# Performance work log

Measured on AMD Instinct MI355X. Metric: run time of the kernel, lower is better.

Reference implementation:

```python
import jax, jax.numpy as jnp
import numpy as np

HEADS = 16
D_MODEL = 1024
HEAD_DIM = D_MODEL // HEADS


def setup_inputs() -> dict:
    key = jax.random.key(0)
    ks = jax.random.split(key, 11)
    B, S, D = 2, 2048, D_MODEL
    s = 1.0 / np.sqrt(D)
    inp = {
        'Q': jax.random.normal(ks[0], (B, S, D), jnp.float32),
        'K': jax.random.normal(ks[1], (B, S, D), jnp.float32),
        'V': jax.random.normal(ks[2], (B, S, D), jnp.float32),
        'Wq': jax.random.normal(ks[3], (D, D), jnp.float32) * s,
        'Wk': jax.random.normal(ks[4], (D, D), jnp.float32) * s,
        'Wv': jax.random.normal(ks[5], (D, D), jnp.float32) * s,
        'Wo': jax.random.normal(ks[6], (D, D), jnp.float32) * s,
        'bq': jnp.zeros((D,), jnp.float32),
        'bk': jnp.zeros((D,), jnp.float32),
        'bv': jnp.zeros((D,), jnp.float32),
        'bo': jnp.zeros((D,), jnp.float32),
    }
    return inp


def reference(Q, K, V, Wq, Wk, Wv, Wo, bq, bk, bv, bo):
    B, S, D = Q.shape
    H, Dh = HEADS, HEAD_DIM
    # projections (torch Linear: x @ W.T + b)
    q = (Q @ Wq.T + bq).reshape(B, S, H, Dh).transpose(0, 2, 1, 3)  # [B,H,S,Dh]
    k = (K @ Wk.T + bk).reshape(B, S, H, Dh).transpose(0, 2, 1, 3)
    v = (V @ Wv.T + bv).reshape(B, S, H, Dh).transpose(0, 2, 1, 3)
    # naive scaled dot-product attention, scale = 1/sqrt(head_dim)
    scores = jnp.einsum('bhqd,bhkd->bhqk', q, k) / jnp.sqrt(jnp.float32(Dh))
    attn = jax.nn.softmax(scores, axis=-1)
    out = jnp.einsum('bhqk,bhkd->bhqd', attn, v)
    concat = out.transpose(0, 2, 1, 3).reshape(B, S, D)
    return concat @ Wo.T + bo
```

## Files before the change

kernel.cpp:

```cpp
#include <hip/hip_runtime.h>
#include <hip/hip_bf16.h>


#define SEQ     2048
#define DMODEL  1024
#define NHEADS  16
#define DH      64
#define MROWS   4096
#define M1      (1024*1024)
#define M4      (4*1024*1024)
#define SCQ     0.18033688f

typedef __hip_bfloat16 bf16;
typedef __attribute__((ext_vector_type(8))) short  short8;
typedef __attribute__((ext_vector_type(4))) float  f32x4;

__device__ __forceinline__ bf16 f2b(float x) { return __float2bfloat16(x); }
__device__ __forceinline__ float u2f(unsigned short u) {
    union { unsigned int i; float f; } x; x.i = ((unsigned int)u) << 16; return x.f;
}
__device__ __forceinline__ f32x4 mfma16(short8 a, short8 b, f32x4 c) {
    return __builtin_amdgcn_mfma_f32_16x16x32_bf16(a, b, c, 0, 0, 0);
}
__device__ __forceinline__ unsigned pk2(float a, float b) {
    union { __hip_bfloat162 h; unsigned u; } x;
    x.h = __float22bfloat162_rn(float2{a, b});
    return x.u;
}
__device__ __forceinline__ short8 pk8(float4 a, float4 b) {
    union { short8 s; unsigned u[4]; } x;
    x.u[0] = pk2(a.x, a.y); x.u[1] = pk2(a.z, a.w);
    x.u[2] = pk2(b.x, b.y); x.u[3] = pk2(b.z, b.w);
    return x.s;
}
__device__ __forceinline__ float fexp2(float x) {
    return __builtin_amdgcn_exp2f(x);
}
#define GLDS(g, l) __builtin_amdgcn_global_load_lds( \
    (const __attribute__((address_space(1))) void*)(g), \
    (__attribute__((address_space(3))) void*)(l), 16, 0, 0)

__global__ __launch_bounds__(256) void cvt_all(
    const float* __restrict__ Wq, const float* __restrict__ Wk,
    const float* __restrict__ Wv, const float* __restrict__ Wo,
    const float* __restrict__ Q,  const float* __restrict__ K,
    const float* __restrict__ V,  bf16* __restrict__ dst)
{
    const size_t gid = (size_t)blockIdx.x * 256 + threadIdx.x;
    const size_t e0 = gid * 8;
    const float* s;
    if (e0 < (size_t)4 * M1) {
        const float* w[4] = {Wq, Wk, Wv, Wo};
        s = w[e0 >> 20] + (e0 & (M1 - 1));
    } else {
        const float* a[4] = {nullptr, Q, K, V};
        s = a[e0 >> 22] + (e0 & (M4 - 1));
    }
    float4 x = *(const float4*)s, y = *(const float4*)(s + 4);
    *(short8*)((short*)dst + e0) = pk8(x, y);
}

__global__ __launch_bounds__(256) void cvt_w(
    const float* __restrict__ W0, const float* __restrict__ W1,
    const float* __restrict__ W2, const float* __restrict__ W3,
    bf16* __restrict__ dst)
{
    const int gid = blockIdx.x * 256 + threadIdx.x;
    const int t   = gid >> 17;
    const int off = (gid & 131071) * 8;
    const float* srcs[4] = {W0, W1, W2, W3};
    const float* s = srcs[t] + off;
    float4 a = *(const float4*)s, b = *(const float4*)(s + 4);
    *(short8*)((short*)dst + (size_t)gid * 8) = pk8(a, b);
}

__global__ __launch_bounds__(256) void cvt_1(
    const float* __restrict__ X, bf16* __restrict__ D)
{
    const int gid = blockIdx.x * 256 + threadIdx.x;
    const int off = gid * 8;
    float4 a = *(const float4*)(X + off), b = *(const float4*)(X + off + 4);
    *(short8*)((short*)D + off) = pk8(a, b);
}

template <int BN>
__device__ __forceinline__ void gemm_body(
    const bf16* __restrict__ A, const bf16* __restrict__ B,
    const float* __restrict__ bias, void* __restrict__ outp,
    int m0, int n0, int mode, int bias_m, float scale)
{
    __shared__ short As[128 * 32];
    __shared__ short Bs[BN * 32];
    constexpr int NI = BN / 32;

    const int tid  = threadIdx.x;
    const int lane = tid & 63;
    const int wv   = tid >> 6;
    const int wm   = (wv >> 1) * 64;
    const int wn   = (wv & 1) * (BN / 2);
    const int fn   = lane & 15;
    const int fq   = lane >> 4;

    const int srow = lane >> 2;
    const int scol = (lane & 3) * 8;

    const short* Ag = (const short*)A;
    const short* Bg = (const short*)B;

    f32x4 acc[4][NI];
#pragma unroll
    for (int i = 0; i < 4; ++i)
#pragma unroll
        for (int j = 0; j < NI; ++j) acc[i][j] = (f32x4){0.f, 0.f, 0.f, 0.f};

    for (int k0 = 0; k0 < DMODEL; k0 += 32) {
#pragma unroll
        for (int i = 0; i < 2; ++i) {
            const int rr = wv * 32 + i * 16;
            const short* ga = Ag + (size_t)(m0 + rr + srow) * DMODEL + k0 + scol;
            GLDS(ga, As + rr * 32);
        }
#pragma unroll
        for (int i = 0; i < BN / 64; ++i) {
            const int rr = wv * (BN / 4) + i * 16;
            const short* gb = Bg + (size_t)(n0 + rr + srow) * DMODEL + k0 + scol;
            GLDS(gb, Bs + rr * 32);
        }
        __syncthreads();

        short8 af[4], bfr[NI];
#pragma unroll
        for (int im = 0; im < 4; ++im)
            af[im] = *(const short8*)(As + (wm + im * 16 + fn) * 32 + fq * 8);
#pragma unroll
        for (int in = 0; in < NI; ++in)
            bfr[in] = *(const short8*)(Bs + (wn + in * 16 + fn) * 32 + fq * 8);
#pragma unroll
        for (int im = 0; im < 4; ++im)
#pragma unroll
            for (int in = 0; in < NI; ++in)
                acc[im][in] = mfma16(af[im], bfr[in], acc[im][in]);
        __syncthreads();
    }

#pragma unroll
    for (int im = 0; im < 4; ++im) {
#pragma unroll
        for (int in = 0; in < NI; ++in) {
#pragma unroll
            for (int r = 0; r < 4; ++r) {
                const int m = m0 + wm + im * 16 + fq * 4 + r;
                const int n = n0 + wn + in * 16 + fn;
                const float c = (acc[im][in][r] + (bias_m ? bias[m] : bias[n])) * scale;
                if (mode == 0) {
                    ((float*)outp)[(size_t)m * DMODEL + n] = c;
                } else if (mode == 1) {
                    const int b = m >> 11, s = m & (SEQ - 1);
                    const int h = n >> 6,  d = n & (DH - 1);
                    ((bf16*)outp)[(((size_t)(b * NHEADS + h) * SEQ) + s) * DH + d] = f2b(c);
                } else {
                    const int h = m >> 6,  d = m & (DH - 1);
                    const int b = n >> 11, s = n & (SEQ - 1);
                    const int p = s & 31;
                    const int sp = (s & ~31) | ((p & 12) << 1) | ((p & 16) >> 2) | (p & 3);
                    ((bf16*)outp)[(((size_t)(b * NHEADS + h) * DH) + d) * SEQ + sp] = f2b(c);
                }
            }
        }
    }
}

__global__ __launch_bounds__(256, 3) void gemm_one(
    const bf16* A, const bf16* B, const float* bias, void* out,
    int mode, int bias_m, float scale)
{
    gemm_body<128>(A, B, bias, out, blockIdx.x * 128, blockIdx.y * 128,
                   mode, bias_m, scale);
}

__global__ __launch_bounds__(256, 3) void gemm_fin(
    const bf16* A, const bf16* B, const float* bias, void* out)
{
    gemm_body<64>(A, B, bias, out, blockIdx.x * 128, blockIdx.y * 64, 0, 0, 1.f);
}

__global__ __launch_bounds__(256, 3) void gemm_qkv(
    const bf16* Qb, const bf16* Kb, const bf16* Vb, const bf16* Wb,
    const float* bq, const float* bk, const float* bv,
    bf16* qp, bf16* kp, bf16* vp)
{
    const int blk = blockIdx.x;
    const int z = blk >> 8, t = blk & 255;
    if (z == 0)
        gemm_body<128>(Qb, Wb,          bq, qp, (t >> 3) * 128, (t & 7) * 128, 1, 0, SCQ);
    else if (z == 1)
        gemm_body<128>(Kb, Wb + M1,     bk, kp, (t >> 3) * 128, (t & 7) * 128, 1, 0, 1.f);
    else
        gemm_body<128>(Wb + 2 * M1, Vb, bv, vp, (t >> 5) * 128, (t & 31) * 128, 2, 1, 1.f);
}

__global__ __launch_bounds__(512, 4) void attn_fused(
    const bf16* __restrict__ q,
    const bf16* __restrict__ k,
    const bf16* __restrict__ vt,
    bf16* __restrict__ out)
{
    __shared__ short LB[32768];

    const int tid  = threadIdx.x;
    const int wave = tid >> 6;
    const int half = wave >> 2;
    const int w4   = wave & 3;
    const int lane = tid & 63;
    const int n    = lane & 15;
    const int quad = lane >> 4;

    const int blk  = blockIdx.x;
    const int xcd  = blk & 7;
    const int rest = blk >> 3;
    const int qt   = rest & 15;
    const int bh   = ((rest >> 4) << 3) | xcd;
    const int q0w  = qt * 128 + w4 * 32;
    const int kt0  = half * 16;

    const bf16* qhead = q  + (size_t)bh * SEQ * DH;
    const bf16* khead = k  + (size_t)bh * SEQ * DH;
    const bf16* vhead = vt + (size_t)bh * DH * SEQ;

    short* Kb0 = LB + half * 16384;
    short* Vb0 = LB + half * 16384 + 8192;

    short8 qf[2][2];
#pragma unroll
    for (int qg = 0; qg < 2; ++qg) {
        const short* qr = (const short*)(qhead + (size_t)(q0w + qg * 16 + n) * DH);
        qf[qg][0] = *(const short8*)(qr + quad * 8);
        qf[qg][1] = *(const short8*)(qr + 32 + quad * 8);
    }

    const short8 onesv = {(short)0x3F80, (short)0x3F80, (short)0x3F80, (short)0x3F80,
                          (short)0x3F80, (short)0x3F80, (short)0x3F80, (short)0x3F80};
    const f32x4 Zv = (f32x4){0.f, 0.f, 0.f, 0.f};

    f32x4 O[4][2];
#pragma unroll
    for (int gd = 0; gd < 4; ++gd)
#pragma unroll
        for (int qg = 0; qg < 2; ++qg) O[gd][qg] = Zv;
    f32x4 lacc[2][2] = {{Zv, Zv}, {Zv, Zv}};

    const int srow = lane >> 3;
    const int schk = (lane & 7) ^ srow;
    const int off0 = ((quad       ^ (n & 7)) * 8);
    const int off1 = (((4 + quad) ^ (n & 7)) * 8);

    auto stage = [&](int kt, int buf) {
        const int kbase = kt * 64;
#pragma unroll
        for (int i = 0; i < 2; ++i) {
            const int r = w4 * 16 + i * 8 + srow;
            const char* gk = (const char*)(khead + (size_t)(kbase + r) * DH) + schk * 16;
            const char* gv = (const char*)(vhead + (size_t)r * SEQ + kbase) + schk * 16;
            GLDS(gk, Kb0 + buf * 4096 + (w4 * 16 + i * 8) * 64);
            GLDS(gv, Vb0 + buf * 4096 + (w4 * 16 + i * 8) * 64);
        }
    };

    auto tile_body = [&](const short* KtB, const short* VtB) {
        f32x4 st[4][2];
#pragma unroll
        for (int g = 0; g < 4; ++g) {
            const short* kr = KtB + (g * 16 + n) * 64;
            short8 kf0 = *(const short8*)(kr + off0);
            short8 kf1 = *(const short8*)(kr + off1);
#pragma unroll
            for (int qg = 0; qg < 2; ++qg) {
                f32x4 s = mfma16(kf0, qf[qg][0], Zv);
                s = mfma16(kf1, qf[qg][1], s);
                st[g][qg] = s;
            }
        }
        short8 bP[2][2];
#pragma unroll
        for (int t = 0; t < 2; ++t) {
#pragma unroll
            for (int qg = 0; qg < 2; ++qg) {
                union { short8 s8; unsigned u[4]; } bb;
                bb.u[0] = pk2(fexp2(st[2*t][qg][0]),   fexp2(st[2*t][qg][1]));
                bb.u[1] = pk2(fexp2(st[2*t][qg][2]),   fexp2(st[2*t][qg][3]));
                bb.u[2] = pk2(fexp2(st[2*t+1][qg][0]), fexp2(st[2*t+1][qg][1]));
                bb.u[3] = pk2(fexp2(st[2*t+1][qg][2]), fexp2(st[2*t+1][qg][3]));
                bP[t][qg] = bb.s8;
                lacc[t][qg] = mfma16(onesv, bP[t][qg], lacc[t][qg]);
            }
        }
#pragma unroll
        for (int gd = 0; gd < 4; ++gd) {
            const short* vr = VtB + (gd * 16 + n) * 64;
            short8 vf0 = *(const short8*)(vr + off0);
            short8 vf1 = *(const short8*)(vr + off1);
#pragma unroll
            for (int qg = 0; qg < 2; ++qg) {
                O[gd][qg] = mfma16(vf0, bP[0][qg], O[gd][qg]);
                O[gd][qg] = mfma16(vf1, bP[1][qg], O[gd][qg]);
            }
        }
    };

    stage(kt0, 0);
#pragma unroll 1
    for (int t = 0; t < 16; t += 2) {
        __syncthreads();
        stage(kt0 + t + 1, 1);
        tile_body(Kb0, Vb0);
        __syncthreads();
        if (t + 2 < 16) stage(kt0 + t + 2, 0);
        tile_body(Kb0 + 4096, Vb0 + 4096);
    }

    float* scr = (float*)LB + (size_t)(w4 * 64 + lane) * 34;
    const float l0 = lacc[0][0][0] + lacc[1][0][0];
    const float l1 = lacc[0][1][0] + lacc[1][1][0];

    __syncthreads();
    if (half == 1) {
#pragma unroll
        for (int gd = 0; gd < 4; ++gd)
#pragma unroll
            for (int qg = 0; qg < 2; ++qg) {
                *(float2*)(scr + (gd * 2 + qg) * 4)     = float2{O[gd][qg][0], O[gd][qg][1]};
                *(float2*)(scr + (gd * 2 + qg) * 4 + 2) = float2{O[gd][qg][2], O[gd][qg][3]};
            }
        *(float2*)(scr + 32) = float2{l0, l1};
    }
    __syncthreads();
    if (half == 0) {
        const float2 lo = *(const float2*)(scr + 32);
        const float inv0 = 1.0f / (l0 + lo.x);
        const float inv1 = 1.0f / (l1 + lo.y);
        const int b = bh >> 4;
        const int h = bh & (NHEADS - 1);
#pragma unroll
        for (int gd = 0; gd < 4; ++gd) {
#pragma unroll
            for (int qg = 0; qg < 2; ++qg) {
                const float iv = qg ? inv1 : inv0;
                float2 a = *(const float2*)(scr + (gd * 2 + qg) * 4);
                float2 c = *(const float2*)(scr + (gd * 2 + qg) * 4 + 2);
                const int s = q0w + qg * 16 + n;
                uint2 o;
                o.x = pk2((O[gd][qg][0] + a.x) * iv, (O[gd][qg][1] + a.y) * iv);
                o.y = pk2((O[gd][qg][2] + c.x) * iv, (O[gd][qg][3] + c.y) * iv);
                *(uint2*)(out + ((size_t)(b * SEQ + s)) * DMODEL + h * DH + gd * 16 + quad * 4) = o;
            }
        }
    }
}

__global__ __launch_bounds__(256) void attn_mfma(
    const bf16* __restrict__ q,
    const bf16* __restrict__ k,
    const bf16* __restrict__ vt,
    bf16* __restrict__ out)
{
    __shared__ short Kt[2][64 * 64];
    __shared__ short Vt[2][64 * 64];

    const int tid  = threadIdx.x;
    const int wave = tid >> 6;
    const int lane = tid & 63;
    const int n    = lane & 15;
    const int quad = lane >> 4;

    const int blk  = blockIdx.x;
    const int xcd  = blk & 7;
    const int rest = blk >> 3;
    const int qt   = rest & 15;
    const int bh   = ((rest >> 4) << 3) | xcd;
    const int q0w  = qt * 128 + wave * 32;

    const bf16* qhead = q  + (size_t)bh * SEQ * DH;
    const bf16* khead = k  + (size_t)bh * SEQ * DH;
    const bf16* vhead = vt + (size_t)bh * DH * SEQ;

    short8 qf[2][2];
#pragma unroll
    for (int qg = 0; qg < 2; ++qg) {
        const short* qr = (const short*)(qhead + (size_t)(q0w + qg * 16 + n) * DH);
        qf[qg][0] = *(const short8*)(qr + quad * 8);
        qf[qg][1] = *(const short8*)(qr + 32 + quad * 8);
    }

    const short8 onesv = {(short)0x3F80, (short)0x3F80, (short)0x3F80, (short)0x3F80,
                          (short)0x3F80, (short)0x3F80, (short)0x3F80, (short)0x3F80};
    const f32x4 Zv = (f32x4){0.f, 0.f, 0.f, 0.f};

    f32x4 O[4][2];
#pragma unroll
    for (int gd = 0; gd < 4; ++gd)
#pragma unroll
        for (int qg = 0; qg < 2; ++qg) O[gd][qg] = Zv;
    f32x4 lacc[2] = {Zv, Zv};

    const int srow = lane >> 3;
    const int schk = (lane & 7) ^ srow;
    const int off0 = ((quad       ^ (n & 7)) * 8);
    const int off1 = (((4 + quad) ^ (n & 7)) * 8);

    auto stage = [&](int kt, int buf) {
        const int kbase = kt * 64;
#pragma unroll
        for (int i = 0; i < 2; ++i) {
            const int r = wave * 16 + i * 8 + srow;
            const char* gk = (const char*)(khead + (size_t)(kbase + r) * DH) + schk * 16;
            const char* gv = (const char*)(vhead + (size_t)r * SEQ + kbase) + schk * 16;
            GLDS(gk, Kt[buf] + (wave * 16 + i * 8) * 64);
            GLDS(gv, Vt[buf] + (wave * 16 + i * 8) * 64);
        }
    };

    auto tile_body = [&](const short* KtB, const short* VtB) {
        f32x4 st[4][2];
#pragma unroll
        for (int g = 0; g < 4; ++g) {
            const short* kr = KtB + (g * 16 + n) * 64;
            short8 kf0 = *(const short8*)(kr + off0);
            short8 kf1 = *(const short8*)(kr + off1);
#pragma unroll
            for (int qg = 0; qg < 2; ++qg) {
                f32x4 s = mfma16(kf0, qf[qg][0], Zv);
                s = mfma16(kf1, qf[qg][1], s);
                st[g][qg] = s;
            }
        }
        short8 bP[2][2];
#pragma unroll
        for (int t = 0; t < 2; ++t) {
#pragma unroll
            for (int qg = 0; qg < 2; ++qg) {
                union { short8 s8; unsigned u[4]; } bb;
                bb.u[0] = pk2(fexp2(st[2*t][qg][0]),   fexp2(st[2*t][qg][1]));
                bb.u[1] = pk2(fexp2(st[2*t][qg][2]),   fexp2(st[2*t][qg][3]));
                bb.u[2] = pk2(fexp2(st[2*t+1][qg][0]), fexp2(st[2*t+1][qg][1]));
                bb.u[3] = pk2(fexp2(st[2*t+1][qg][2]), fexp2(st[2*t+1][qg][3]));
                bP[t][qg] = bb.s8;
                lacc[qg] = mfma16(onesv, bP[t][qg], lacc[qg]);
            }
        }
#pragma unroll
        for (int gd = 0; gd < 4; ++gd) {
            const short* vr = VtB + (gd * 16 + n) * 64;
            short8 vf0 = *(const short8*)(vr + off0);
            short8 vf1 = *(const short8*)(vr + off1);
#pragma unroll
            for (int qg = 0; qg < 2; ++qg) {
                O[gd][qg] = mfma16(vf0, bP[0][qg], O[gd][qg]);
                O[gd][qg] = mfma16(vf1, bP[1][qg], O[gd][qg]);
            }
        }
    };

    stage(0, 0);
#pragma unroll 1
    for (int kt = 0; kt < SEQ / 64; kt += 2) {
        __syncthreads();
        stage(kt + 1, 1);
        tile_body(Kt[0], Vt[0]);
        __syncthreads();
        if (kt + 2 < SEQ / 64) stage(kt + 2, 0);
        tile_body(Kt[1], Vt[1]);
    }

    const float inv0 = 1.0f / lacc[0][0];
    const float inv1 = 1.0f / lacc[1][0];
    const int b = bh >> 4;
    const int h = bh & (NHEADS - 1);
#pragma unroll
    for (int gd = 0; gd < 4; ++gd) {
#pragma unroll
        for (int qg = 0; qg < 2; ++qg) {
            const float iv = qg ? inv1 : inv0;
            const int s = q0w + qg * 16 + n;
            uint2 o;
            o.x = pk2(O[gd][qg][0] * iv, O[gd][qg][1] * iv);
            o.y = pk2(O[gd][qg][2] * iv, O[gd][qg][3] * iv);
            *(uint2*)(out + ((size_t)(b * SEQ + s)) * DMODEL + h * DH + gd * 16 + quad * 4) = o;
        }
    }
}

extern "C" void kernel_launch(void* const* d_in, const int* in_sizes, int n_in,
                              void* d_out, int out_size, void* d_ws, size_t ws_size,
                              hipStream_t stream) {
    const float* Q  = (const float*)d_in[0];
    const float* K  = (const float*)d_in[1];
    const float* V  = (const float*)d_in[2];
    const float* Wq = (const float*)d_in[3];
    const float* Wk = (const float*)d_in[4];
    const float* Wv = (const float*)d_in[5];
    const float* Wo = (const float*)d_in[6];
    const float* bq = (const float*)d_in[7];
    const float* bk = (const float*)d_in[8];
    const float* bv = (const float*)d_in[9];
    const float* bo = (const float*)d_in[10];

    bf16* kp = (bf16*)d_out;
    bf16* vp = kp + M4;

    dim3 bb(256);
    dim3 gqk(MROWS / 128, DMODEL / 128);
    dim3 gvv(DMODEL / 128, MROWS / 128);
    dim3 gfin(MROWS / 128, DMODEL / 64);

    if (ws_size >= (size_t)40 * 1024 * 1024) {
        bf16* Wb = (bf16*)d_ws;
        bf16* Qb = Wb + 4 * M1;
        bf16* Kb = Qb + M4;
        bf16* Vb = Kb + M4;
        bf16* qp = Vb + M4;
        bf16* ao = Qb;

        cvt_all<<<8192, bb, 0, stream>>>(Wq, Wk, Wv, Wo, Q, K, V, Wb);
        gemm_qkv<<<768, bb, 0, stream>>>(Qb, Kb, Vb, Wb, bq, bk, bv, qp, kp, vp);
        attn_fused<<<512, 512, 0, stream>>>(qp, kp, vp, ao);
        gemm_fin<<<gfin, bb, 0, stream>>>(ao, Wb + 3 * M1, bo, d_out);
    } else {
        bf16* Wb = (bf16*)d_ws;
        bf16* Xb = Wb + 4 * M1;
        bf16* qp = Xb + M4;
        bf16* ao = Xb;

        cvt_w<<<2048, bb, 0, stream>>>(Wq, Wk, Wv, Wo, Wb);
        cvt_1<<<2048, bb, 0, stream>>>(Q, Xb);
        gemm_one<<<gqk, bb, 0, stream>>>(Xb, Wb, bq, qp, 1, 0, SCQ);
        cvt_1<<<2048, bb, 0, stream>>>(K, Xb);
        gemm_one<<<gqk, bb, 0, stream>>>(Xb, Wb + M1, bk, kp, 1, 0, 1.f);
        cvt_1<<<2048, bb, 0, stream>>>(V, Xb);
        gemm_one<<<gvv, bb, 0, stream>>>(Wb + 2 * M1, Xb, bv, vp, 2, 1, 1.f);
        attn_mfma<<<512, bb, 0, stream>>>(qp, kp, vp, ao);
        gemm_fin<<<gfin, bb, 0, stream>>>(ao, Wb + 3 * M1, bo, d_out);
    }
}
```

Before: 211.9 us.

## Software-pipeline attention loop: overlap QK/exp of next tile with PV of previous

Splits K and V staging into separate async loads and restructures the attention inner loop so that the QK^T and exp2 step for tile t runs alongside the PV and row-sum MFMAs for tile t-1. V is now fetched one stage later than K, with a prologue and epilogue to fill and drain the pipeline. The aim is to interleave the transcendental and pack work with MFMA work and to hide load latency. In exchange it keeps two sets of P fragments live, which raises register pressure and may lower occupancy.

```diff
diff --git a/kernel.cpp b/kernel.cpp
--- a/kernel.cpp
+++ b/kernel.cpp
@@ -16,9 +16,6 @@
 typedef __attribute__((ext_vector_type(4))) float  f32x4;
 
 __device__ __forceinline__ bf16 f2b(float x) { return __float2bfloat16(x); }
-__device__ __forceinline__ float u2f(unsigned short u) {
-    union { unsigned int i; float f; } x; x.i = ((unsigned int)u) << 16; return x.f;
-}
 __device__ __forceinline__ f32x4 mfma16(short8 a, short8 b, f32x4 c) {
     return __builtin_amdgcn_mfma_f32_16x16x32_bf16(a, b, c, 0, 0, 0);
 }
@@ -254,45 +251,61 @@
     const int off0 = ((quad       ^ (n & 7)) * 8);
     const int off1 = (((4 + quad) ^ (n & 7)) * 8);
 
-    auto stage = [&](int kt, int buf) {
+    auto stageK = [&](int kt, int buf) {
         const int kbase = kt * 64;
 #pragma unroll
         for (int i = 0; i < 2; ++i) {
             const int r = w4 * 16 + i * 8 + srow;
             const char* gk = (const char*)(khead + (size_t)(kbase + r) * DH) + schk * 16;
+            GLDS(gk, Kb0 + buf * 4096 + (w4 * 16 + i * 8) * 64);
+        }
+    };
+    auto stageV = [&](int kt, int buf) {
+        const int kbase = kt * 64;
+#pragma unroll
+        for (int i = 0; i < 2; ++i) {
+            const int r = w4 * 16 + i * 8 + srow;
             const char* gv = (const char*)(vhead + (size_t)r * SEQ + kbase) + schk * 16;
-            GLDS(gk, Kb0 + buf * 4096 + (w4 * 16 + i * 8) * 64);
             GLDS(gv, Vb0 + buf * 4096 + (w4 * 16 + i * 8) * 64);
         }
     };
 
-    auto tile_body = [&](const short* KtB, const short* VtB) {
-        f32x4 st[4][2];
-#pragma unroll
-        for (int g = 0; g < 4; ++g) {
-            const short* kr = KtB + (g * 16 + n) * 64;
-            short8 kf0 = *(const short8*)(kr + off0);
-            short8 kf1 = *(const short8*)(kr + off1);
-#pragma unroll
-            for (int qg = 0; qg < 2; ++qg) {
-                f32x4 s = mfma16(kf0, qf[qg][0], Zv);
-                s = mfma16(kf1, qf[qg][1], s);
-                st[g][qg] = s;
-            }
-        }
-        short8 bP[2][2];
-#pragma unroll
-        for (int t = 0; t < 2; ++t) {
+    auto xph = [&](int t, short8 (&bPc)[2][2]) {
+        const short* KtB = Kb0 + (t & 1) * 4096;
+#pragma unroll
+        for (int tt = 0; tt < 2; ++tt) {
+            f32x4 st[2][2];
+#pragma unroll
+            for (int g2 = 0; g2 < 2; ++g2) {
+                const int g = tt * 2 + g2;
+                const short* kr = KtB + (g * 16 + n) * 64;
+                short8 kf0 = *(const short8*)(kr + off0);
+                short8 kf1 = *(const short8*)(kr + off1);
+#pragma unroll
+                for (int qg = 0; qg < 2; ++qg) {
+                    f32x4 s = mfma16(kf0, qf[qg][0], Zv);
+                    s = mfma16(kf1, qf[qg][1], s);
+                    st[g2][qg] = s;
+                }
+            }
 #pragma unroll
             for (int qg = 0; qg < 2; ++qg) {
                 union { short8 s8; unsigned u[4]; } bb;
-                bb.u[0] = pk2(fexp2(st[2*t][qg][0]),   fexp2(st[2*t][qg][1]));
-                bb.u[1] = pk2(fexp2(st[2*t][qg][2]),   fexp2(st[2*t][qg][3]));
-                bb.u[2] = pk2(fexp2(st[2*t+1][qg][0]), fexp2(st[2*t+1][qg][1]));
-                bb.u[3] = pk2(fexp2(st[2*t+1][qg][2]), fexp2(st[2*t+1][qg][3]));
-                bP[t][qg] = bb.s8;
-                lacc[t][qg] = mfma16(onesv, bP[t][qg], lacc[t][qg]);
-            }
+                bb.u[0] = pk2(fexp2(st[0][qg][0]), fexp2(st[0][qg][1]));
+                bb.u[1] = pk2(fexp2(st[0][qg][2]), fexp2(st[0][qg][3]));
+                bb.u[2] = pk2(fexp2(st[1][qg][0]), fexp2(st[1][qg][1]));
+                bb.u[3] = pk2(fexp2(st[1][qg][2]), fexp2(st[1][qg][3]));
+                bPc[tt][qg] = bb.s8;
+            }
+        }
+    };
+
+    auto yph = [&](int t, short8 (&bPp)[2][2]) {
+        const short* VtB = Vb0 + (t & 1) * 4096;
+#pragma unroll
+        for (int qg = 0; qg < 2; ++qg) {
+            lacc[0][qg] = mfma16(onesv, bPp[0][qg], lacc[0][qg]);
+            lacc[1][qg] = mfma16(onesv, bPp[1][qg], lacc[1][qg]);
         }
 #pragma unroll
         for (int gd = 0; gd < 4; ++gd) {
@@ -301,22 +314,40 @@
             short8 vf1 = *(const short8*)(vr + off1);
 #pragma unroll
             for (int qg = 0; qg < 2; ++qg) {
-                O[gd][qg] = mfma16(vf0, bP[0][qg], O[gd][qg]);
-                O[gd][qg] = mfma16(vf1, bP[1][qg], O[gd][qg]);
+                O[gd][qg] = mfma16(vf0, bPp[0][qg], O[gd][qg]);
+                O[gd][qg] = mfma16(vf1, bPp[1][qg], O[gd][qg]);
             }
         }
     };
 
-    stage(kt0, 0);
+    short8 bPA[2][2], bPB[2][2];
+
+    stageK(kt0, 0);
+
+    __syncthreads();
+    stageK(kt0 + 1, 1);
+    stageV(kt0, 0);
+    xph(0, bPA);
+
 #pragma unroll 1
-    for (int t = 0; t < 16; t += 2) {
+    for (int t = 1; t < 15; t += 2) {
         __syncthreads();
-        stage(kt0 + t + 1, 1);
-        tile_body(Kb0, Vb0);
+        stageK(kt0 + t + 1, (t + 1) & 1);
+        stageV(kt0 + t, t & 1);
+        xph(t, bPB);
+        yph(t - 1, bPA);
         __syncthreads();
-        if (t + 2 < 16) stage(kt0 + t + 2, 0);
-        tile_body(Kb0 + 4096, Vb0 + 4096);
-    }
+        stageK(kt0 + t + 2, (t + 2) & 1);
+        stageV(kt0 + t + 1, (t + 1) & 1);
+        xph(t + 1, bPA);
+        yph(t, bPB);
+    }
+    __syncthreads();
+    stageV(kt0 + 15, 1);
+    xph(15, bPB);
+    yph(14, bPA);
+    __syncthreads();
+    yph(15, bPB);
 
     float* scr = (float*)LB + (size_t)(w4 * 64 + lane) * 34;
     const float l0 = lacc[0][0][0] + lacc[1][0][0];
```

Measured after the change: 225.7 us. 6.5% more time.

## Load K/V tiles straight into registers instead of staging through LDS

Applied to the files above, without the earlier changes.

The attention kernel stops staging K and V tiles into shared memory with global_load_lds and double buffering. Each wave now loads its own K/V fragments from global memory into registers and prefetches the next tile while the current one is computed, which removes the per-tile __syncthreads and LDS traffic. Shared memory shrinks to the small reduction scratch buffer, and the occupancy hint in launch_bounds drops from 4 to 2 blocks per CU. In exchange, K/V data that waves used to share through LDS is fetched redundantly by every wave from global memory or cache, and register pressure rises.

```diff
diff --git a/kernel.cpp b/kernel.cpp
--- a/kernel.cpp
+++ b/kernel.cpp
@@ -16,9 +16,6 @@
 typedef __attribute__((ext_vector_type(4))) float  f32x4;
 
 __device__ __forceinline__ bf16 f2b(float x) { return __float2bfloat16(x); }
-__device__ __forceinline__ float u2f(unsigned short u) {
-    union { unsigned int i; float f; } x; x.i = ((unsigned int)u) << 16; return x.f;
-}
 __device__ __forceinline__ f32x4 mfma16(short8 a, short8 b, f32x4 c) {
     return __builtin_amdgcn_mfma_f32_16x16x32_bf16(a, b, c, 0, 0, 0);
 }
@@ -199,13 +196,13 @@
         gemm_body<128>(Wb + 2 * M1, Vb, bv, vp, (t >> 5) * 128, (t & 31) * 128, 2, 1, 1.f);
 }
 
-__global__ __launch_bounds__(512, 4) void attn_fused(
+__global__ __launch_bounds__(512, 2) void attn_fused(
     const bf16* __restrict__ q,
     const bf16* __restrict__ k,
     const bf16* __restrict__ vt,
     bf16* __restrict__ out)
 {
-    __shared__ short LB[32768];
+    __shared__ float SCR[256 * 34];
 
     const int tid  = threadIdx.x;
     const int wave = tid >> 6;
@@ -223,19 +220,18 @@
     const int q0w  = qt * 128 + w4 * 32;
     const int kt0  = half * 16;
 
-    const bf16* qhead = q  + (size_t)bh * SEQ * DH;
-    const bf16* khead = k  + (size_t)bh * SEQ * DH;
-    const bf16* vhead = vt + (size_t)bh * DH * SEQ;
-
-    short* Kb0 = LB + half * 16384;
-    short* Vb0 = LB + half * 16384 + 8192;
-
-    short8 qf[2][2];
-#pragma unroll
-    for (int qg = 0; qg < 2; ++qg) {
-        const short* qr = (const short*)(qhead + (size_t)(q0w + qg * 16 + n) * DH);
-        qf[qg][0] = *(const short8*)(qr + quad * 8);
-        qf[qg][1] = *(const short8*)(qr + 32 + quad * 8);
+    const short* qh = (const short*)(q  + (size_t)bh * SEQ * DH);
+    const short* kh = (const short*)(k  + (size_t)bh * SEQ * DH);
+    const short* vh = (const short*)(vt + (size_t)bh * DH * SEQ);
+
+    short8 qf00, qf01, qf10, qf11;
+    {
+        const short* qr0 = qh + (size_t)(q0w + n) * DH;
+        qf00 = *(const short8*)(qr0 + quad * 8);
+        qf01 = *(const short8*)(qr0 + 32 + quad * 8);
+        const short* qr1 = qh + (size_t)(q0w + 16 + n) * DH;
+        qf10 = *(const short8*)(qr1 + quad * 8);
+        qf11 = *(const short8*)(qr1 + 32 + quad * 8);
     }
 
     const short8 onesv = {(short)0x3F80, (short)0x3F80, (short)0x3F80, (short)0x3F80,
@@ -247,80 +243,86 @@
     for (int gd = 0; gd < 4; ++gd)
 #pragma unroll
         for (int qg = 0; qg < 2; ++qg) O[gd][qg] = Zv;
-    f32x4 lacc[2][2] = {{Zv, Zv}, {Zv, Zv}};
-
-    const int srow = lane >> 3;
-    const int schk = (lane & 7) ^ srow;
-    const int off0 = ((quad       ^ (n & 7)) * 8);
-    const int off1 = (((4 + quad) ^ (n & 7)) * 8);
-
-    auto stage = [&](int kt, int buf) {
-        const int kbase = kt * 64;
-#pragma unroll
-        for (int i = 0; i < 2; ++i) {
-            const int r = w4 * 16 + i * 8 + srow;
-            const char* gk = (const char*)(khead + (size_t)(kbase + r) * DH) + schk * 16;
-            const char* gv = (const char*)(vhead + (size_t)r * SEQ + kbase) + schk * 16;
-            GLDS(gk, Kb0 + buf * 4096 + (w4 * 16 + i * 8) * 64);
-            GLDS(gv, Vb0 + buf * 4096 + (w4 * 16 + i * 8) * 64);
-        }
-    };
-
-    auto tile_body = [&](const short* KtB, const short* VtB) {
+    f32x4 lc0 = Zv, lc1 = Zv;
+
+    const short* kp[4];
+    const short* vp[4];
+#pragma unroll
+    for (int g = 0; g < 4; ++g)
+        kp[g] = kh + (size_t)(kt0 * 64 + g * 16 + n) * 64 + quad * 8;
+#pragma unroll
+    for (int gd = 0; gd < 4; ++gd)
+        vp[gd] = vh + (size_t)(gd * 16 + n) * SEQ + kt0 * 64 + quad * 8;
+
+    short8 Kr[4][2];
+    short8 Vr[4][2];
+
+#pragma unroll
+    for (int g = 0; g < 4; ++g) {
+        Kr[g][0] = *(const short8*)(kp[g]);
+        Kr[g][1] = *(const short8*)(kp[g] + 32);
+    }
+#pragma unroll
+    for (int gd = 0; gd < 4; ++gd) {
+        Vr[gd][0] = *(const short8*)(vp[gd]);
+        Vr[gd][1] = *(const short8*)(vp[gd] + 32);
+    }
+
+#pragma unroll 1
+    for (int t = 0; t < 16; ++t) {
         f32x4 st[4][2];
 #pragma unroll
         for (int g = 0; g < 4; ++g) {
-            const short* kr = KtB + (g * 16 + n) * 64;
-            short8 kf0 = *(const short8*)(kr + off0);
-            short8 kf1 = *(const short8*)(kr + off1);
-#pragma unroll
-            for (int qg = 0; qg < 2; ++qg) {
-                f32x4 s = mfma16(kf0, qf[qg][0], Zv);
-                s = mfma16(kf1, qf[qg][1], s);
-                st[g][qg] = s;
-            }
-        }
-        short8 bP[2][2];
-#pragma unroll
-        for (int t = 0; t < 2; ++t) {
+            f32x4 s0 = mfma16(Kr[g][0], qf00, Zv);
+            st[g][0] = mfma16(Kr[g][1], qf01, s0);
+            f32x4 s1 = mfma16(Kr[g][0], qf10, Zv);
+            st[g][1] = mfma16(Kr[g][1], qf11, s1);
+        }
+        if (t < 15) {
+#pragma unroll
+            for (int g = 0; g < 4; ++g) {
+                kp[g] += 64 * 64;
+                Kr[g][0] = *(const short8*)(kp[g]);
+                Kr[g][1] = *(const short8*)(kp[g] + 32);
+            }
+        }
+        short8 P[2][2];
+#pragma unroll
+        for (int tt = 0; tt < 2; ++tt) {
 #pragma unroll
             for (int qg = 0; qg < 2; ++qg) {
                 union { short8 s8; unsigned u[4]; } bb;
-                bb.u[0] = pk2(fexp2(st[2*t][qg][0]),   fexp2(st[2*t][qg][1]));
-                bb.u[1] = pk2(fexp2(st[2*t][qg][2]),   fexp2(st[2*t][qg][3]));
-                bb.u[2] = pk2(fexp2(st[2*t+1][qg][0]), fexp2(st[2*t+1][qg][1]));
-                bb.u[3] = pk2(fexp2(st[2*t+1][qg][2]), fexp2(st[2*t+1][qg][3]));
-                bP[t][qg] = bb.s8;
-                lacc[t][qg] = mfma16(onesv, bP[t][qg], lacc[t][qg]);
-            }
-        }
+                bb.u[0] = pk2(fexp2(st[2*tt][qg][0]),   fexp2(st[2*tt][qg][1]));
+                bb.u[1] = pk2(fexp2(st[2*tt][qg][2]),   fexp2(st[2*tt][qg][3]));
+                bb.u[2] = pk2(fexp2(st[2*tt+1][qg][0]), fexp2(st[2*tt+1][qg][1]));
+                bb.u[3] = pk2(fexp2(st[2*tt+1][qg][2]), fexp2(st[2*tt+1][qg][3]));
+                P[tt][qg] = bb.s8;
+            }
+        }
+        lc0 = mfma16(onesv, P[0][0], lc0);
+        lc1 = mfma16(onesv, P[0][1], lc1);
+        lc0 = mfma16(onesv, P[1][0], lc0);
+        lc1 = mfma16(onesv, P[1][1], lc1);
 #pragma unroll
         for (int gd = 0; gd < 4; ++gd) {
-            const short* vr = VtB + (gd * 16 + n) * 64;
-            short8 vf0 = *(const short8*)(vr + off0);
-            short8 vf1 = *(const short8*)(vr + off1);
-#pragma unroll
-            for (int qg = 0; qg < 2; ++qg) {
-                O[gd][qg] = mfma16(vf0, bP[0][qg], O[gd][qg]);
-                O[gd][qg] = mfma16(vf1, bP[1][qg], O[gd][qg]);
-            }
-        }
-    };
-
-    stage(kt0, 0);
-#pragma unroll 1
-    for (int t = 0; t < 16; t += 2) {
-        __syncthreads();
-        stage(kt0 + t + 1, 1);
-        tile_body(Kb0, Vb0);
-        __syncthreads();
-        if (t + 2 < 16) stage(kt0 + t + 2, 0);
-        tile_body(Kb0 + 4096, Vb0 + 4096);
-    }
-
-    float* scr = (float*)LB + (size_t)(w4 * 64 + lane) * 34;
-    const float l0 = lacc[0][0][0] + lacc[1][0][0];
-    const float l1 = lacc[0][1][0] + lacc[1][1][0];
+            O[gd][0] = mfma16(Vr[gd][0], P[0][0], O[gd][0]);
+            O[gd][0] = mfma16(Vr[gd][1], P[1][0], O[gd][0]);
+            O[gd][1] = mfma16(Vr[gd][0], P[0][1], O[gd][1]);
+            O[gd][1] = mfma16(Vr[gd][1], P[1][1], O[gd][1]);
+        }
+        if (t < 15) {
+#pragma unroll
+            for (int gd = 0; gd < 4; ++gd) {
+                vp[gd] += 64;
+                Vr[gd][0] = *(const short8*)(vp[gd]);
+                Vr[gd][1] = *(const short8*)(vp[gd] + 32);
+            }
+        }
+    }
+
+    float* scr = SCR + (size_t)(w4 * 64 + lane) * 34;
+    const float l0 = lc0[0];
+    const float l1 = lc1[0];
 
     __syncthreads();
     if (half == 1) {
```

Result: slower. 289.3 us (+36.6%).

## Restructure attention into single-wave blocks with async K/V pipelining, retile output GEMM

Applied to the files above, without the earlier changes.

The fused attention kernel now runs one 64-thread wave per block. Each wave handles 64 query rows over the full key range, so the cross-half LDS reduction and __syncthreads are gone. K and V tiles are double-buffered through global_load_lds with explicit vmcnt waits, and the MFMA section runs at raised priority. The output GEMM switches to 128x128 tiles and the Q/K projection tile order is swapped. The wave-level kernel trades block-level parallelism and LDS sharing for fewer barriers, but it uses more registers per wave and each block loads its own K/V tiles.

```diff
diff --git a/kernel.cpp b/kernel.cpp
--- a/kernel.cpp
+++ b/kernel.cpp
@@ -16,9 +16,6 @@
 typedef __attribute__((ext_vector_type(4))) float  f32x4;
 
 __device__ __forceinline__ bf16 f2b(float x) { return __float2bfloat16(x); }
-__device__ __forceinline__ float u2f(unsigned short u) {
-    union { unsigned int i; float f; } x; x.i = ((unsigned int)u) << 16; return x.f;
-}
 __device__ __forceinline__ f32x4 mfma16(short8 a, short8 b, f32x4 c) {
     return __builtin_amdgcn_mfma_f32_16x16x32_bf16(a, b, c, 0, 0, 0);
 }
@@ -181,7 +178,7 @@
 __global__ __launch_bounds__(256, 3) void gemm_fin(
     const bf16* A, const bf16* B, const float* bias, void* out)
 {
-    gemm_body<64>(A, B, bias, out, blockIdx.x * 128, blockIdx.y * 64, 0, 0, 1.f);
+    gemm_body<128>(A, B, bias, out, blockIdx.x * 128, blockIdx.y * 128, 0, 0, 1.f);
 }
 
 __global__ __launch_bounds__(256, 3) void gemm_qkv(
@@ -192,47 +189,39 @@
     const int blk = blockIdx.x;
     const int z = blk >> 8, t = blk & 255;
     if (z == 0)
-        gemm_body<128>(Qb, Wb,          bq, qp, (t >> 3) * 128, (t & 7) * 128, 1, 0, SCQ);
+        gemm_body<128>(Qb, Wb,          bq, qp, (t & 31) * 128, (t >> 5) * 128, 1, 0, SCQ);
     else if (z == 1)
-        gemm_body<128>(Kb, Wb + M1,     bk, kp, (t >> 3) * 128, (t & 7) * 128, 1, 0, 1.f);
+        gemm_body<128>(Kb, Wb + M1,     bk, kp, (t & 31) * 128, (t >> 5) * 128, 1, 0, 1.f);
     else
         gemm_body<128>(Wb + 2 * M1, Vb, bv, vp, (t >> 5) * 128, (t & 31) * 128, 2, 1, 1.f);
 }
 
-__global__ __launch_bounds__(512, 4) void attn_fused(
+__global__ __launch_bounds__(64, 2) void attn_fused(
     const bf16* __restrict__ q,
     const bf16* __restrict__ k,
     const bf16* __restrict__ vt,
     bf16* __restrict__ out)
 {
-    __shared__ short LB[32768];
-
-    const int tid  = threadIdx.x;
-    const int wave = tid >> 6;
-    const int half = wave >> 2;
-    const int w4   = wave & 3;
-    const int lane = tid & 63;
+    __shared__ short LB[16384];
+
+    const int lane = threadIdx.x & 63;
     const int n    = lane & 15;
     const int quad = lane >> 4;
 
     const int blk  = blockIdx.x;
     const int xcd  = blk & 7;
     const int rest = blk >> 3;
-    const int qt   = rest & 15;
-    const int bh   = ((rest >> 4) << 3) | xcd;
-    const int q0w  = qt * 128 + w4 * 32;
-    const int kt0  = half * 16;
+    const int qt   = rest & 31;
+    const int bh   = ((rest >> 5) << 3) | xcd;
+    const int q0w  = qt * 64;
 
     const bf16* qhead = q  + (size_t)bh * SEQ * DH;
     const bf16* khead = k  + (size_t)bh * SEQ * DH;
     const bf16* vhead = vt + (size_t)bh * DH * SEQ;
 
-    short* Kb0 = LB + half * 16384;
-    short* Vb0 = LB + half * 16384 + 8192;
-
-    short8 qf[2][2];
-#pragma unroll
-    for (int qg = 0; qg < 2; ++qg) {
+    short8 qf[4][2];
+#pragma unroll
+    for (int qg = 0; qg < 4; ++qg) {
         const short* qr = (const short*)(qhead + (size_t)(q0w + qg * 16 + n) * DH);
         qf[qg][0] = *(const short8*)(qr + quad * 8);
         qf[qg][1] = *(const short8*)(qr + 32 + quad * 8);
@@ -242,57 +231,83 @@
                           (short)0x3F80, (short)0x3F80, (short)0x3F80, (short)0x3F80};
     const f32x4 Zv = (f32x4){0.f, 0.f, 0.f, 0.f};
 
-    f32x4 O[4][2];
+    f32x4 O[4][4];
 #pragma unroll
     for (int gd = 0; gd < 4; ++gd)
 #pragma unroll
-        for (int qg = 0; qg < 2; ++qg) O[gd][qg] = Zv;
-    f32x4 lacc[2][2] = {{Zv, Zv}, {Zv, Zv}};
+        for (int qg = 0; qg < 4; ++qg) O[gd][qg] = Zv;
+    f32x4 lc[4];
+#pragma unroll
+    for (int qg = 0; qg < 4; ++qg) lc[qg] = Zv;
 
     const int srow = lane >> 3;
     const int schk = (lane & 7) ^ srow;
     const int off0 = ((quad       ^ (n & 7)) * 8);
     const int off1 = (((4 + quad) ^ (n & 7)) * 8);
 
-    auto stage = [&](int kt, int buf) {
-        const int kbase = kt * 64;
-#pragma unroll
-        for (int i = 0; i < 2; ++i) {
-            const int r = w4 * 16 + i * 8 + srow;
-            const char* gk = (const char*)(khead + (size_t)(kbase + r) * DH) + schk * 16;
-            const char* gv = (const char*)(vhead + (size_t)r * SEQ + kbase) + schk * 16;
-            GLDS(gk, Kb0 + buf * 4096 + (w4 * 16 + i * 8) * 64);
-            GLDS(gv, Vb0 + buf * 4096 + (w4 * 16 + i * 8) * 64);
-        }
+    const char* gk0 = (const char*)khead + (size_t)srow * 128  + schk * 16;
+    const char* gv0 = (const char*)vhead + (size_t)srow * 4096 + schk * 16;
+
+    auto stageK = [&](int buf) {
+#pragma unroll
+        for (int i = 0; i < 8; ++i)
+            GLDS(gk0 + i * 1024, LB + buf * 4096 + i * 512);
+        gk0 += 8192;
     };
-
-    auto tile_body = [&](const short* KtB, const short* VtB) {
-        f32x4 st[4][2];
-#pragma unroll
-        for (int g = 0; g < 4; ++g) {
-            const short* kr = KtB + (g * 16 + n) * 64;
-            short8 kf0 = *(const short8*)(kr + off0);
-            short8 kf1 = *(const short8*)(kr + off1);
-#pragma unroll
-            for (int qg = 0; qg < 2; ++qg) {
-                f32x4 s = mfma16(kf0, qf[qg][0], Zv);
-                s = mfma16(kf1, qf[qg][1], s);
-                st[g][qg] = s;
-            }
-        }
-        short8 bP[2][2];
-#pragma unroll
-        for (int t = 0; t < 2; ++t) {
-#pragma unroll
-            for (int qg = 0; qg < 2; ++qg) {
+    auto stageV = [&](int buf) {
+#pragma unroll
+        for (int i = 0; i < 8; ++i)
+            GLDS(gv0 + (size_t)i * 32768, LB + 8192 + buf * 4096 + i * 512);
+        gv0 += 128;
+    };
+
+    stageK(0);
+    stageV(0);
+
+#pragma unroll 1
+    for (int t = 0; t < 32; ++t) {
+        if (t < 31) {
+            stageK((t + 1) & 1);
+            stageV((t + 1) & 1);
+            asm volatile("s_waitcnt vmcnt(16)" ::: "memory");
+        } else {
+            asm volatile("s_waitcnt vmcnt(0)" ::: "memory");
+        }
+
+        const short* KtB = LB + (t & 1) * 4096;
+        const short* VtB = LB + 8192 + (t & 1) * 4096;
+
+        short8 P[2][4];
+#pragma unroll
+        for (int tt = 0; tt < 2; ++tt) {
+            f32x4 st[2][4];
+#pragma unroll
+            for (int g2 = 0; g2 < 2; ++g2) {
+                const short* kr = KtB + ((tt * 2 + g2) * 16 + n) * 64;
+                short8 kf0 = *(const short8*)(kr + off0);
+                short8 kf1 = *(const short8*)(kr + off1);
+#pragma unroll
+                for (int qg = 0; qg < 4; ++qg) {
+                    f32x4 s = mfma16(kf0, qf[qg][0], Zv);
+                    st[g2][qg] = mfma16(kf1, qf[qg][1], s);
+                }
+            }
+#pragma unroll
+            for (int qg = 0; qg < 4; ++qg) {
                 union { short8 s8; unsigned u[4]; } bb;
-                bb.u[0] = pk2(fexp2(st[2*t][qg][0]),   fexp2(st[2*t][qg][1]));
-                bb.u[1] = pk2(fexp2(st[2*t][qg][2]),   fexp2(st[2*t][qg][3]));
-                bb.u[2] = pk2(fexp2(st[2*t+1][qg][0]), fexp2(st[2*t+1][qg][1]));
-                bb.u[3] = pk2(fexp2(st[2*t+1][qg][2]), fexp2(st[2*t+1][qg][3]));
-                bP[t][qg] = bb.s8;
-                lacc[t][qg] = mfma16(onesv, bP[t][qg], lacc[t][qg]);
-            }
+                bb.u[0] = pk2(fexp2(st[0][qg][0]), fexp2(st[0][qg][1]));
+                bb.u[1] = pk2(fexp2(st[0][qg][2]), fexp2(st[0][qg][3]));
+                bb.u[2] = pk2(fexp2(st[1][qg][0]), fexp2(st[1][qg][1]));
+                bb.u[3] = pk2(fexp2(st[1][qg][2]), fexp2(st[1][qg][3]));
+                P[tt][qg] = bb.s8;
+            }
+        }
+
+        __builtin_amdgcn_s_setprio(1);
+#pragma unroll
+        for (int qg = 0; qg < 4; ++qg) {
+            lc[qg] = mfma16(onesv, P[0][qg], lc[qg]);
+            lc[qg] = mfma16(onesv, P[1][qg], lc[qg]);
         }
 #pragma unroll
         for (int gd = 0; gd < 4; ++gd) {
@@ -300,59 +315,29 @@
             short8 vf0 = *(const short8*)(vr + off0);
             short8 vf1 = *(const short8*)(vr + off1);
 #pragma unroll
-            for (int qg = 0; qg < 2; ++qg) {
-                O[gd][qg] = mfma16(vf0, bP[0][qg], O[gd][qg]);
-                O[gd][qg] = mfma16(vf1, bP[1][qg], O[gd][qg]);
-            }
-        }
-    };
-
-    stage(kt0, 0);
-#pragma unroll 1
-    for (int t = 0; t < 16; t += 2) {
-        __syncthreads();
-        stage(kt0 + t + 1, 1);
-        tile_body(Kb0, Vb0);
-        __syncthreads();
-        if (t + 2 < 16) stage(kt0 + t + 2, 0);
-        tile_body(Kb0 + 4096, Vb0 + 4096);
-    }
-
-    float* scr = (float*)LB + (size_t)(w4 * 64 + lane) * 34;
-    const float l0 = lacc[0][0][0] + lacc[1][0][0];
-    const float l1 = lacc[0][1][0] + lacc[1][1][0];
-
-    __syncthreads();
-    if (half == 1) {
-#pragma unroll
-        for (int gd = 0; gd < 4; ++gd)
-#pragma unroll
-            for (int qg = 0; qg < 2; ++qg) {
-                *(float2*)(scr + (gd * 2 + qg) * 4)     = float2{O[gd][qg][0], O[gd][qg][1]};
-                *(float2*)(scr + (gd * 2 + qg) * 4 + 2) = float2{O[gd][qg][2], O[gd][qg][3]};
-            }
-        *(float2*)(scr + 32) = float2{l0, l1};
-    }
-    __syncthreads();
-    if (half == 0) {
-        const float2 lo = *(const float2*)(scr + 32);
-        const float inv0 = 1.0f / (l0 + lo.x);
-        const float inv1 = 1.0f / (l1 + lo.y);
-        const int b = bh >> 4;
-        const int h = bh & (NHEADS - 1);
-#pragma unroll
-        for (int gd = 0; gd < 4; ++gd) {
-#pragma unroll
-            for (int qg = 0; qg < 2; ++qg) {
-                const float iv = qg ? inv1 : inv0;
-                float2 a = *(const float2*)(scr + (gd * 2 + qg) * 4);
-                float2 c = *(const float2*)(scr + (gd * 2 + qg) * 4 + 2);
-                const int s = q0w + qg * 16 + n;
-                uint2 o;
-                o.x = pk2((O[gd][qg][0] + a.x) * iv, (O[gd][qg][1] + a.y) * iv);
-                o.y = pk2((O[gd][qg][2] + c.x) * iv, (O[gd][qg][3] + c.y) * iv);
-                *(uint2*)(out + ((size_t)(b * SEQ + s)) * DMODEL + h * DH + gd * 16 + quad * 4) = o;
-            }
+            for (int qg = 0; qg < 4; ++qg) {
+                O[gd][qg] = mfma16(vf0, P[0][qg], O[gd][qg]);
+                O[gd][qg] = mfma16(vf1, P[1][qg], O[gd][qg]);
+            }
+        }
+        __builtin_amdgcn_s_setprio(0);
+    }
+
+    float inv[4];
+#pragma unroll
+    for (int qg = 0; qg < 4; ++qg) inv[qg] = 1.0f / lc[qg][0];
+    const int b = bh >> 4;
+    const int h = bh & (NHEADS - 1);
+#pragma unroll
+    for (int gd = 0; gd < 4; ++gd) {
+#pragma unroll
+        for (int qg = 0; qg < 4; ++qg) {
+            const float iv = inv[qg];
+            const int s = q0w + qg * 16 + n;
+            uint2 o;
+            o.x = pk2(O[gd][qg][0] * iv, O[gd][qg][1] * iv);
+            o.y = pk2(O[gd][qg][2] * iv, O[gd][qg][3] * iv);
+            *(uint2*)(out + ((size_t)(b * SEQ + s)) * DMODEL + h * DH + gd * 16 + quad * 4) = o;
         }
     }
 }
@@ -510,7 +495,7 @@
     dim3 bb(256);
     dim3 gqk(MROWS / 128, DMODEL / 128);
     dim3 gvv(DMODEL / 128, MROWS / 128);
-    dim3 gfin(MROWS / 128, DMODEL / 64);
+    dim3 gfin(MROWS / 128, DMODEL / 128);
 
     if (ws_size >= (size_t)40 * 1024 * 1024) {
         bf16* Wb = (bf16*)d_ws;
@@ -522,7 +507,7 @@
 
         cvt_all<<<8192, bb, 0, stream>>>(Wq, Wk, Wv, Wo, Q, K, V, Wb);
         gemm_qkv<<<768, bb, 0, stream>>>(Qb, Kb, Vb, Wb, bq, bk, bv, qp, kp, vp);
-        attn_fused<<<512, 512, 0, stream>>>(qp, kp, vp, ao);
+        attn_fused<<<1024, 64, 0, stream>>>(qp, kp, vp, ao);
         gemm_fin<<<gfin, bb, 0, stream>>>(ao, Wb + 3 * M1, bo, d_out);
     } else {
         bf16* Wb = (bf16*)d_ws;
```

New measurement: 239.4 us. +13.0%, slower.
